# Optimization experiments

Hardware: AMD Instinct MI355X
Metric: run time of the kernel (lower is better)

The kernel has to match this reference:

```python
import jax, jax.numpy as jnp
import numpy as np

B, N, C = 2, 2048, 768
H, HD = 12, 64
HID = 3072
LN_EPS = 1e-5
POL_EPS = 1e-6


def _layer_norm(x, g, b):
    m = jnp.mean(x, axis=-1, keepdims=True)
    v = jnp.mean(jnp.square(x - m), axis=-1, keepdims=True)
    return (x - m) * jax.lax.rsqrt(v + LN_EPS) * g + b


def _softmax_with_policy(attn, policy):
    # attn: [B,H,N,N], policy: [B,N,1]
    n = attn.shape[-1]
    ap = policy.reshape(policy.shape[0], 1, 1, n)  # [B,1,1,N]
    eye = jnp.eye(n, dtype=ap.dtype)[None, None]   # [1,1,N,N]
    ap = ap + (1.0 - ap) * eye                     # always attend to self
    attn = attn - jnp.max(attn, axis=-1, keepdims=True)
    attn = jnp.exp(attn.astype(jnp.float32)) * ap.astype(jnp.float32)
    attn = (attn + POL_EPS / n) / (jnp.sum(attn, axis=-1, keepdims=True) + POL_EPS)
    return attn


def setup_inputs() -> dict:
    key = jax.random.key(0)
    ks = jax.random.split(key, 12)
    s = lambda fan_in: 1.0 / np.sqrt(fan_in)
    x = jax.random.normal(ks[0], (B, N, C), dtype=jnp.float32)
    policy = (jax.random.uniform(ks[1], (B, N, 1)) > 0.5).astype(jnp.float32)
    return {
        "x": x,
        "policy": policy,
        "ln1_g": jnp.ones((C,), jnp.float32),
        "ln1_b": jnp.zeros((C,), jnp.float32),
        "qkv_w": jax.random.uniform(ks[2], (3 * H * HD, C), jnp.float32, -s(C), s(C)),
        "proj_w": jax.random.uniform(ks[3], (C, H * HD), jnp.float32, -s(H * HD), s(H * HD)),
        "proj_b": jnp.zeros((C,), jnp.float32),
        "ln2_g": jnp.ones((C,), jnp.float32),
        "ln2_b": jnp.zeros((C,), jnp.float32),
        "fc1_w": jax.random.uniform(ks[4], (HID, C), jnp.float32, -s(C), s(C)),
        "fc1_b": jnp.zeros((HID,), jnp.float32),
        "fc2_w": jax.random.uniform(ks[5], (C, HID), jnp.float32, -s(HID), s(HID)),
        "fc2_b": jnp.zeros((C,), jnp.float32),
    }


def reference(x, policy, ln1_g, ln1_b, qkv_w, proj_w, proj_b, ln2_g, ln2_b, fc1_w, fc1_b, fc2_w, fc2_b):
    b, n, c = x.shape
    scale = HD ** -0.5
    # --- attention branch (pre-LN) ---
    h = _layer_norm(x, ln1_g, ln1_b)
    qkv = (h @ qkv_w.T).reshape(b, n, 3, H, HD).transpose(2, 0, 3, 1, 4)  # [3,B,H,N,hd]
    q, k, v = qkv[0], qkv[1], qkv[2]
    attn = jnp.einsum("bhqd,bhkd->bhqk", q * scale, k)
    attn = _softmax_with_policy(attn, policy).astype(x.dtype)
    o = jnp.einsum("bhqk,bhkd->bhqd", attn, v).transpose(0, 2, 1, 3).reshape(b, n, H * HD)
    x = x + (o @ proj_w.T + proj_b)  # skip_lam = 1.0, dropout/drop_path = identity
    # --- MLP branch (pre-LN) ---
    h = _layer_norm(x, ln2_g, ln2_b)
    h = jax.nn.gelu(h @ fc1_w.T + fc1_b, approximate=False)  # torch nn.GELU = exact erf
    x = x + (h @ fc2_w.T + fc2_b)
    return x
```

## Files before the change

### kernel.cpp

```cpp
#include <hip/hip_runtime.h>

typedef unsigned short u16;
typedef unsigned int u32;
typedef float f32x4 __attribute__((ext_vector_type(4)));
typedef float f32x16 __attribute__((ext_vector_type(16)));
typedef __bf16 bf16x8 __attribute__((ext_vector_type(8)));
typedef u16 u16x4v __attribute__((ext_vector_type(4)));
typedef u32 u32x2 __attribute__((ext_vector_type(2)));
typedef u32 u32x4 __attribute__((ext_vector_type(4)));

#define NHEAD 12
#define NN 2048
#define CC 768

#define GLOBAL_AS __attribute__((address_space(1)))
#define LDS_AS __attribute__((address_space(3)))

__device__ __forceinline__ u16 tobf(float f) {
  __bf16 h = (__bf16)f;
  return __builtin_bit_cast(u16, h);
}
__device__ __forceinline__ float bf2f(u16 h) {
  u32 u = ((u32)h) << 16;
  return __builtin_bit_cast(float, u);
}
__device__ __forceinline__ void plswap(u32& a, u32& b) {
  asm volatile("v_permlane32_swap_b32 %0, %1" : "+v"(a), "+v"(b));
}
__device__ __forceinline__ void plswapf(float& a, float& b) {
  asm volatile("v_permlane32_swap_b32 %0, %1" : "+v"(a), "+v"(b));
}

#define N4_QKV 442368
#define N4_PROJ 147456
#define N4_FC 589824
__global__ __launch_bounds__(256) void cvt4_kernel(
    const float* __restrict__ a, const float* __restrict__ b,
    const float* __restrict__ c, const float* __restrict__ d,
    u16* __restrict__ oa, u16* __restrict__ ob, u16* __restrict__ oc,
    u16* __restrict__ od) {
  int i = blockIdx.x * 256 + threadIdx.x;
  const float* src;
  u16* dst;
  if (i < N4_QKV) {
    src = a; dst = oa;
  } else if (i < N4_QKV + N4_PROJ) {
    i -= N4_QKV; src = b; dst = ob;
  } else if (i < N4_QKV + N4_PROJ + N4_FC) {
    i -= N4_QKV + N4_PROJ; src = c; dst = oc;
  } else {
    i -= N4_QKV + N4_PROJ + N4_FC; src = d; dst = od;
    if (i >= N4_FC) return;
  }
  float4 v = ((const float4*)src)[i];
  u16x4v o = {tobf(v.x), tobf(v.y), tobf(v.z), tobf(v.w)};
  ((u16x4v*)dst)[i] = o;
}

__global__ __launch_bounds__(256) void ln_kernel(const float* __restrict__ x,
                                                 const float* __restrict__ gw,
                                                 const float* __restrict__ bw,
                                                 u16* __restrict__ out) {
  int row = blockIdx.x * 4 + (threadIdx.x >> 6);
  int lane = threadIdx.x & 63;
  const float* xr = x + (size_t)row * CC + lane * 12;
  float v[12];
  *(float4*)&v[0] = *(const float4*)(xr + 0);
  *(float4*)&v[4] = *(const float4*)(xr + 4);
  *(float4*)&v[8] = *(const float4*)(xr + 8);
  float s = 0.f, sq = 0.f;
#pragma unroll
  for (int j = 0; j < 12; ++j) { s += v[j]; sq += v[j] * v[j]; }
#pragma unroll
  for (int o = 1; o < 64; o <<= 1) { s += __shfl_xor(s, o); sq += __shfl_xor(sq, o); }
  float mean = s * (1.f / CC);
  float var = sq * (1.f / CC) - mean * mean;
  float rs = rsqrtf(var + 1e-5f);
  u16 ob[12];
#pragma unroll
  for (int j = 0; j < 12; ++j) {
    int c = lane * 12 + j;
    ob[j] = tobf((v[j] - mean) * rs * gw[c] + bw[c]);
  }
  u32* orow = (u32*)(out + (size_t)row * CC + lane * 12);
#pragma unroll
  for (int j = 0; j < 6; ++j) orow[j] = (u32)ob[2 * j] | ((u32)ob[2 * j + 1] << 16);
}

template <int BM, int OB, int HASB, int ACT, int RES>
__global__ __launch_bounds__(256) void gemm_kernel(
    const u16* __restrict__ A, const u16* __restrict__ Bw,
    const float* __restrict__ bias, const float* __restrict__ res,
    void* __restrict__ Cout, int M, int N, int K) {
  constexpr int MW = BM / 2;
  constexpr int MF = MW / 16;
  __shared__ __align__(16) u16 Alds[BM * 64];
  __shared__ __align__(16) u16 Blds[128 * 64];
  const int tid = threadIdx.x;
  const int lane = tid & 63, wave = tid >> 6;
  const int l15 = lane & 15, g = lane >> 4;
  const int bm = blockIdx.x * BM, bn = blockIdx.y * 128;
  const int wm = (wave >> 1) * MW, wn = (wave & 1) * 64;
  f32x4 acc[MF][4] = {};

  for (int kt = 0; kt < K; kt += 64) {
#pragma unroll
    for (int i = 0; i < BM / 32; ++i) {
      int ob_ = i * 4096 + wave * 1024;
      int lb = ob_ + lane * 16;
      int row = lb >> 7;
      int cb = (lb & 127) ^ ((row & 7) << 4);
      const u16* sa = A + (size_t)(bm + row) * K + kt + (cb >> 1);
      __builtin_amdgcn_global_load_lds((const GLOBAL_AS void*)sa,
                                       (LDS_AS void*)(Alds + (ob_ >> 1)), 16, 0, 0);
    }
#pragma unroll
    for (int i = 0; i < 4; ++i) {
      int ob_ = i * 4096 + wave * 1024;
      int lb = ob_ + lane * 16;
      int row = lb >> 7;
      int cb = (lb & 127) ^ ((row & 7) << 4);
      const u16* sb = Bw + (size_t)(bn + row) * K + kt + (cb >> 1);
      __builtin_amdgcn_global_load_lds((const GLOBAL_AS void*)sb,
                                       (LDS_AS void*)(Blds + (ob_ >> 1)), 16, 0, 0);
    }
    __syncthreads();
#pragma unroll
    for (int ks = 0; ks < 2; ++ks) {
      bf16x8 af[MF], bfr[4];
#pragma unroll
      for (int mi = 0; mi < MF; ++mi) {
        int row = wm + mi * 16 + l15;
        int cb = (ks * 64 + g * 16) ^ ((row & 7) << 4);
        af[mi] = *(const bf16x8*)&Alds[row * 64 + (cb >> 1)];
      }
#pragma unroll
      for (int ni = 0; ni < 4; ++ni) {
        int row = wn + ni * 16 + l15;
        int cb = (ks * 64 + g * 16) ^ ((row & 7) << 4);
        bfr[ni] = *(const bf16x8*)&Blds[row * 64 + (cb >> 1)];
      }
#pragma unroll
      for (int mi = 0; mi < MF; ++mi)
#pragma unroll
        for (int ni = 0; ni < 4; ++ni)
          acc[mi][ni] = __builtin_amdgcn_mfma_f32_16x16x32_bf16(af[mi], bfr[ni],
                                                                acc[mi][ni], 0, 0, 0);
    }
    __syncthreads();
  }
#pragma unroll
  for (int mi = 0; mi < MF; ++mi) {
#pragma unroll
    for (int ni = 0; ni < 4; ++ni) {
      int col = bn + wn + ni * 16 + l15;
      float bs = HASB ? bias[col] : 0.f;
#pragma unroll
      for (int r = 0; r < 4; ++r) {
        int rowm = bm + wm + mi * 16 + g * 4 + r;
        float v = acc[mi][ni][r] + bs;
        if (ACT) v = 0.5f * v * (1.f + erff(v * 0.70710678118654752f));
        if (RES) v += res[(size_t)rowm * N + col];
        if (OB)
          ((u16*)Cout)[(size_t)rowm * N + col] = tobf(v);
        else
          ((float*)Cout)[(size_t)rowm * N + col] = v;
      }
    }
  }
}

__global__ __launch_bounds__(256) void vsum_kernel(const u16* __restrict__ qkv,
                                                   float* __restrict__ vs) {
  int bh = blockIdx.x, q4 = blockIdx.y;
  int b = bh / NHEAD, h = bh % NHEAD;
  int d = threadIdx.x & 63, part = threadIdx.x >> 6;
  float s = 0.f;
  for (int n = q4 * 512 + part; n < q4 * 512 + 512; n += 4)
    s += bf2f(qkv[(size_t)(b * NN + n) * 2304 + 2 * CC + h * 64 + d]);
  __shared__ float red[256];
  red[threadIdx.x] = s;
  __syncthreads();
  if (threadIdx.x < 64) {
    float t = red[threadIdx.x] + red[threadIdx.x + 64] + red[threadIdx.x + 128] +
              red[threadIdx.x + 192];
    vs[q4 * (24 * 64) + bh * 64 + threadIdx.x] = t;
  }
}

#define SCL2E 0.18033688f
#define TRRD(dst, addr, OFF) \
  asm volatile("ds_read_b64_tr_b16 %0, %1 offset:" OFF : "=v"(dst) : "v"(addr))
#define VMW(N)                                          \
  asm volatile("s_waitcnt vmcnt(" #N ")" ::: "memory"); \
  __builtin_amdgcn_sched_barrier(0);

__global__ __launch_bounds__(256) void attn32_kernel(const u16* __restrict__ qkv,
                                                     const float* __restrict__ policy,
                                                     float* __restrict__ partO,
                                                     float* __restrict__ partlm) {
  __shared__ __align__(16) u16 Vlds[4][2][2048];
  __shared__ u16 PolB[NN];
  __shared__ float alf[4][32];
  const int bh = blockIdx.y, b = bh / NHEAD, h = bh % NHEAD;
  const int qt = blockIdx.x >> 1, half = blockIdx.x & 1;
  const int tid = threadIdx.x, lane = tid & 63, w = tid >> 6;
  const int l31 = lane & 31, hp = lane >> 5, b4 = (lane >> 4) & 1, l15 = lane & 15;
  const int q0 = qt * 128 + w * 32;
  const int kv0 = half * 1024;

  bf16x8 qf0, qf1, qf2, qf3;
  {
    const u16* qp = qkv + (size_t)(b * NN + q0 + l31) * 2304 + h * 64 + 8 * hp;
#pragma unroll
    for (int ds = 0; ds < 4; ++ds) {
      bf16x8 r = *(const bf16x8*)(qp + ds * 16);
      bf16x8 o;
#pragma unroll
      for (int j = 0; j < 8; ++j) o[j] = (__bf16)((float)r[j] * SCL2E);
      if (ds == 0) qf0 = o; else if (ds == 1) qf1 = o; else if (ds == 2) qf2 = o; else qf3 = o;
    }
  }

  const u16* kptr = qkv + (size_t)(b * NN + kv0 + l31) * 2304 + CC + h * 64 + 8 * hp;
  const u16* vsrc[4];
#pragma unroll
  for (int c = 0; c < 4; ++c) {
    int L = c * 64 + lane;
    int idx0 = L * 8;
    int s0 = idx0 & 15, jj = (idx0 >> 4) & 3, b4v = (idx0 >> 6) & 1,
        pv = (idx0 >> 7) & 1, hv = (idx0 >> 8) & 1, dtv = (idx0 >> 9) & 1,
        mkv = (idx0 >> 10) & 1;
    int key = mkv * 16 + 8 * hv + 4 * pv + jj;
    int d0 = dtv * 32 + 16 * b4v + s0;
    vsrc[c] = qkv + (size_t)(b * NN + kv0 + key) * 2304 + 2 * CC + h * 64 + d0;
  }

#define LOADK(R0, R1, R2, R3)              \
  {                                        \
    R0 = *(const bf16x8*)(kptr);           \
    R1 = *(const bf16x8*)(kptr + 16);      \
    R2 = *(const bf16x8*)(kptr + 32);      \
    R3 = *(const bf16x8*)(kptr + 48);      \
    kptr += 73728;                         \
  }
#define STAGEV(BUF)                                                              \
  {                                                                              \
    _Pragma("unroll") for (int c = 0; c < 4; ++c) {                              \
      __builtin_amdgcn_global_load_lds((const GLOBAL_AS void*)vsrc[c],           \
                                       (LDS_AS void*)&Vlds[w][BUF][c * 512], 16, \
                                       0, 0);                                    \
      vsrc[c] += 73728;                                                          \
    }                                                                            \
  }

  bf16x8 kA0, kA1, kA2, kA3, kB0, kB1, kB2, kB3;
  STAGEV(0);
  LOADK(kA0, kA1, kA2, kA3);
  {
    float4 p0 = *(const float4*)&policy[b * NN + tid * 8];
    float4 p1 = *(const float4*)&policy[b * NN + tid * 8 + 4];
    u16x4v a = {tobf(p0.x), tobf(p0.y), tobf(p0.z), tobf(p0.w)};
    u16x4v c2 = {tobf(p1.x), tobf(p1.y), tobf(p1.z), tobf(p1.w)};
    *(u16x4v*)&PolB[tid * 8] = a;
    *(u16x4v*)&PolB[tid * 8 + 4] = c2;
  }
  __syncthreads();

  float m_cur = -3.0e38f, m_true = -3.0e38f, l_run = 0.f;
  f32x16 accd[2] = {};
  const u32 vwb = (u32)(uintptr_t)(LDS_AS u16*)&Vlds[w][0][0] +
                  (u32)(2 * l15 + 128 * b4 + 512 * hp);

  auto tile_body = [&](int T, bf16x8 k0, bf16x8 k1, bf16x8 k2, bf16x8 k3,
                       int bufb) {
    f32x16 sv = {};
    sv = __builtin_amdgcn_mfma_f32_32x32x16_bf16(k0, qf0, sv, 0, 0, 0);
    sv = __builtin_amdgcn_mfma_f32_32x32x16_bf16(k1, qf1, sv, 0, 0, 0);
    sv = __builtin_amdgcn_mfma_f32_32x32x16_bf16(k2, qf2, sv, 0, 0, 0);
    sv = __builtin_amdgcn_mfma_f32_32x32x16_bf16(k3, qf3, sv, 0, 0, 0);

    u32x2 t00a, t00b, t01a, t01b, t10a, t10b, t11a, t11b;
    {
      u32 vab = vwb + (u32)(bufb * 4096);
      TRRD(t00a, vab, "0");    TRRD(t00b, vab, "256");
      TRRD(t01a, vab, "1024"); TRRD(t01b, vab, "1280");
      TRRD(t10a, vab, "2048"); TRRD(t10b, vab, "2304");
      TRRD(t11a, vab, "3072"); TRRD(t11b, vab, "3328");
    }

    float m01 = fmaxf(sv[0], sv[1]), m23 = fmaxf(sv[2], sv[3]);
    float m45 = fmaxf(sv[4], sv[5]), m67 = fmaxf(sv[6], sv[7]);
    float m89 = fmaxf(sv[8], sv[9]), mab = fmaxf(sv[10], sv[11]);
    float mcd = fmaxf(sv[12], sv[13]), mef = fmaxf(sv[14], sv[15]);
    float tmax = fmaxf(fmaxf(fmaxf(m01, m23), fmaxf(m45, m67)),
                       fmaxf(fmaxf(m89, mab), fmaxf(mcd, mef)));
    {
      float t1 = tmax, t2 = tmax;
      plswapf(t1, t2);
      tmax = fmaxf(t1, t2);
    }
    m_true = fmaxf(m_true, tmax);
    const bool defer = __all(tmax <= m_cur + 8.f);
    const float m_new = defer ? m_cur : fmaxf(m_cur, tmax);

    const int kvg = kv0 + T * 32;
    const bool isdiag = (kvg == q0);
    u16 pb[16];
    float psum = 0.f;
#pragma unroll
    for (int i = 0; i < 4; ++i) {
      u16x4v pq = *(const u16x4v*)&PolB[kvg + 8 * i + 4 * hp];
#pragma unroll
      for (int rq = 0; rq < 4; ++rq) {
        int r = 4 * i + rq;
        float ap = bf2f(pq[rq]);
        if (isdiag) ap = ((8 * i + 4 * hp + rq) == l31) ? 1.f : ap;
        float e = exp2f(sv[r] - m_new) * ap;
        u16 eb = tobf(e);
        psum += bf2f(eb);
        pb[r] = eb;
      }
    }
    {
      float s1 = psum, s2 = psum;
      plswapf(s1, s2);
      psum = s1 + s2;
    }
    if (!defer) {
      float alpha = exp2f(m_cur - m_new);
      l_run = l_run * alpha + psum;
      m_cur = m_new;
      if (lane < 32) alf[w][lane] = alpha;
      float4 aq0 = *(const float4*)&alf[w][4 * hp];
      float4 aq1 = *(const float4*)&alf[w][8 + 4 * hp];
      float4 aq2 = *(const float4*)&alf[w][16 + 4 * hp];
      float4 aq3 = *(const float4*)&alf[w][24 + 4 * hp];
#pragma unroll
      for (int dt = 0; dt < 2; ++dt) {
#pragma unroll
        for (int rq = 0; rq < 4; ++rq) {
          accd[dt][0 + rq] *= ((const float*)&aq0)[rq];
          accd[dt][4 + rq] *= ((const float*)&aq1)[rq];
          accd[dt][8 + rq] *= ((const float*)&aq2)[rq];
          accd[dt][12 + rq] *= ((const float*)&aq3)[rq];
        }
      }
    } else {
      l_run += psum;
    }

    u32 PK0[4], PK1[4];
    PK0[0] = (u32)pb[0] | ((u32)pb[1] << 16);
    PK0[1] = (u32)pb[2] | ((u32)pb[3] << 16);
    PK0[2] = (u32)pb[4] | ((u32)pb[5] << 16);
    PK0[3] = (u32)pb[6] | ((u32)pb[7] << 16);
    PK1[0] = (u32)pb[8] | ((u32)pb[9] << 16);
    PK1[1] = (u32)pb[10] | ((u32)pb[11] << 16);
    PK1[2] = (u32)pb[12] | ((u32)pb[13] << 16);
    PK1[3] = (u32)pb[14] | ((u32)pb[15] << 16);
    plswap(PK0[2], PK0[0]);
    plswap(PK0[3], PK0[1]);
    plswap(PK1[2], PK1[0]);
    plswap(PK1[3], PK1[1]);

    asm volatile("s_waitcnt lgkmcnt(0)" ::: "memory");
    __builtin_amdgcn_sched_barrier(0);

    {
      u32x4 p4 = {PK0[0], PK0[1], PK0[2], PK0[3]};
      bf16x8 pf = __builtin_bit_cast(bf16x8, p4);
      u32x4 v0 = {t00a.x, t00a.y, t00b.x, t00b.y};
      u32x4 v1 = {t01a.x, t01a.y, t01b.x, t01b.y};
      accd[0] = __builtin_amdgcn_mfma_f32_32x32x16_bf16(
          pf, __builtin_bit_cast(bf16x8, v0), accd[0], 0, 0, 0);
      accd[1] = __builtin_amdgcn_mfma_f32_32x32x16_bf16(
          pf, __builtin_bit_cast(bf16x8, v1), accd[1], 0, 0, 0);
    }
    {
      u32x4 p4 = {PK1[0], PK1[1], PK1[2], PK1[3]};
      bf16x8 pf = __builtin_bit_cast(bf16x8, p4);
      u32x4 v0 = {t10a.x, t10a.y, t10b.x, t10b.y};
      u32x4 v1 = {t11a.x, t11a.y, t11b.x, t11b.y};
      accd[0] = __builtin_amdgcn_mfma_f32_32x32x16_bf16(
          pf, __builtin_bit_cast(bf16x8, v0), accd[0], 0, 0, 0);
      accd[1] = __builtin_amdgcn_mfma_f32_32x32x16_bf16(
          pf, __builtin_bit_cast(bf16x8, v1), accd[1], 0, 0, 0);
    }
  };

  for (int tt = 0; tt < 16; ++tt) {
    LOADK(kB0, kB1, kB2, kB3);
    STAGEV(1);
    VMW(8);
    tile_body(2 * tt, kA0, kA1, kA2, kA3, 0);
    if (tt < 15) {
      LOADK(kA0, kA1, kA2, kA3);
      STAGEV(0);
      VMW(8);
    } else {
      VMW(0);
    }
    tile_body(2 * tt + 1, kB0, kB1, kB2, kB3, 1);
  }

  float sr = exp2f(m_cur - m_true);
  if (lane < 32) {
    alf[w][lane] = sr;
    float2 lm = {l_run * sr, m_true};
    *(float2*)&partlm[2 * ((size_t)(half * 24 + bh) * 2048 + q0 + lane)] = lm;
  }
  float4 sq0 = *(const float4*)&alf[w][4 * hp];
  float4 sq1 = *(const float4*)&alf[w][8 + 4 * hp];
  float4 sq2 = *(const float4*)&alf[w][16 + 4 * hp];
  float4 sq3 = *(const float4*)&alf[w][24 + 4 * hp];
  float* pb2 = partO + ((size_t)(half * 24 + bh) * 2048) * 64;
#pragma unroll
  for (int dt = 0; dt < 2; ++dt) {
#pragma unroll
    for (int i = 0; i < 4; ++i) {
      float4 sqv = (i == 0) ? sq0 : (i == 1) ? sq1 : (i == 2) ? sq2 : sq3;
#pragma unroll
      for (int rq = 0; rq < 4; ++rq) {
        int row = q0 + 8 * i + 4 * hp + rq;
        pb2[(size_t)row * 64 + dt * 32 + l31] = accd[dt][4 * i + rq] * ((const float*)&sqv)[rq];
      }
    }
  }
#undef LOADK
#undef STAGEV
}

__global__ __launch_bounds__(256) void merge_kernel(const float* __restrict__ partO,
                                                    const float* __restrict__ partlm,
                                                    const float* __restrict__ vs,
                                                    u16* __restrict__ o) {
  int rr = blockIdx.x * 4 + (threadIdx.x >> 6);
  int lane = threadIdx.x & 63;
  int bh = rr >> 11, q = rr & 2047;
  int b = bh / NHEAD, h = bh % NHEAD;
  const float* O1 = partO + ((size_t)bh * 2048 + q) * 64;
  const float* O2 = partO + ((size_t)(24 + bh) * 2048 + q) * 64;
  float2 lm1 = ((const float2*)partlm)[(size_t)bh * 2048 + q];
  float2 lm2 = ((const float2*)partlm)[(size_t)(24 + bh) * 2048 + q];
  float ms = fmaxf(lm1.y, lm2.y);
  float w1 = exp2f(lm1.y - ms), w2 = exp2f(lm2.y - ms);
  float den = lm1.x * w1 + lm2.x * w2 + 1e-6f;
  float vsv = vs[bh * 64 + lane] + vs[1536 + bh * 64 + lane] +
              vs[3072 + bh * 64 + lane] + vs[4608 + bh * 64 + lane];
  float num = O1[lane] * w1 + O2[lane] * w2 + (1e-6f / 2048.f) * vsv;
  o[((size_t)(b * NN + q)) * CC + h * 64 + lane] = tobf(num / den);
}

extern "C" void kernel_launch(void* const* d_in, const int* in_sizes, int n_in,
                              void* d_out, int out_size, void* d_ws, size_t ws_size,
                              hipStream_t stream) {
  const float* x = (const float*)d_in[0];
  const float* policy = (const float*)d_in[1];
  const float* ln1g = (const float*)d_in[2];
  const float* ln1b = (const float*)d_in[3];
  const float* qkvw = (const float*)d_in[4];
  const float* projw = (const float*)d_in[5];
  const float* projb = (const float*)d_in[6];
  const float* ln2g = (const float*)d_in[7];
  const float* ln2b = (const float*)d_in[8];
  const float* fc1w = (const float*)d_in[9];
  const float* fc1b = (const float*)d_in[10];
  const float* fc2w = (const float*)d_in[11];
  const float* fc2b = (const float*)d_in[12];
  float* out = (float*)d_out;

  char* ws = (char*)d_ws;
  size_t off = 0;
  auto alloc = [&](size_t bytes) {
    void* p = ws + off;
    off = (off + bytes + 255) & ~(size_t)255;
    return p;
  };
  u16* wq = (u16*)alloc((size_t)2304 * 768 * 2);
  u16* wp = (u16*)alloc((size_t)768 * 768 * 2);
  u16* w1 = (u16*)alloc((size_t)3072 * 768 * 2);
  u16* w2 = (u16*)alloc((size_t)768 * 3072 * 2);
  u16* hbuf = (u16*)alloc((size_t)4096 * 768 * 2);
  u16* qkv = (u16*)alloc((size_t)4096 * 2304 * 2);
  u16* obuf = (u16*)alloc((size_t)4096 * 768 * 2);
  float* vs = (float*)alloc((size_t)4 * 24 * 64 * 4);
  size_t unionOff = off;
  float* partO = (float*)alloc((size_t)2 * 24 * 2048 * 64 * 4);
  float* partlm = (float*)alloc((size_t)2 * 24 * 2048 * 2 * 4);
  float* x1 = (float*)(ws + unionOff);
  u16* f1 = qkv;

  cvt4_kernel<<<6912, 256, 0, stream>>>(qkvw, projw, fc1w, fc2w, wq, wp, w1, w2);

  ln_kernel<<<1024, 256, 0, stream>>>(x, ln1g, ln1b, hbuf);
  gemm_kernel<128, 1, 0, 0, 0><<<dim3(32, 18), 256, 0, stream>>>(
      hbuf, wq, nullptr, nullptr, qkv, 4096, 2304, 768);
  vsum_kernel<<<dim3(24, 4), 256, 0, stream>>>(qkv, vs);
  attn32_kernel<<<dim3(32, 24), 256, 0, stream>>>(qkv, policy, partO, partlm);
  merge_kernel<<<12288, 256, 0, stream>>>(partO, partlm, vs, obuf);
  gemm_kernel<64, 0, 1, 0, 1><<<dim3(64, 6), 256, 0, stream>>>(
      obuf, wp, projb, x, x1, 4096, 768, 768);
  ln_kernel<<<1024, 256, 0, stream>>>(x1, ln2g, ln2b, hbuf);
  gemm_kernel<128, 1, 1, 1, 0><<<dim3(32, 24), 256, 0, stream>>>(
      hbuf, w1, fc1b, nullptr, f1, 4096, 3072, 768);
  gemm_kernel<64, 0, 1, 0, 1><<<dim3(64, 6), 256, 0, stream>>>(
      f1, w2, fc2b, x1, out, 4096, 768, 3072);
}
```

Measured before the change: 263.8 us.

## Swizzle GEMM tile order and streamline attention softmax conversions

The GEMM kernel remaps block indices through a modulo-8 swizzle, probably to spread neighbouring tiles across XCDs or improve L2 reuse. In the attention kernel, policy values are kept as fp32 in LDS. The kernel now uses the raw hardware exp2 instruction and packs bf16 pairs with v_cvt_pk_bf16_f32 instead of per-element conversion and shifting. It also reshapes the max reduction tree and forces the main KV loop not to unroll, which lowers code size and register pressure but may cost some scheduling freedom.

```diff
diff --git a/kernel.cpp b/kernel.cpp
--- a/kernel.cpp
+++ b/kernel.cpp
@@ -23,6 +23,11 @@
 __device__ __forceinline__ float bf2f(u16 h) {
   u32 u = ((u32)h) << 16;
   return __builtin_bit_cast(float, u);
+}
+__device__ __forceinline__ u32 cvtpk(float lo, float hi) {
+  u32 r;
+  asm("v_cvt_pk_bf16_f32 %0, %1, %2" : "=v"(r) : "v"(lo), "v"(hi));
+  return r;
 }
 __device__ __forceinline__ void plswap(u32& a, u32& b) {
   asm volatile("v_permlane32_swap_b32 %0, %1" : "+v"(a), "+v"(b));
@@ -99,7 +104,11 @@
   const int tid = threadIdx.x;
   const int lane = tid & 63, wave = tid >> 6;
   const int l15 = lane & 15, g = lane >> 4;
-  const int bm = blockIdx.x * BM, bn = blockIdx.y * 128;
+  const int nx = gridDim.x;
+  const int flat = blockIdx.y * nx + blockIdx.x;
+  const int cpx = (nx * gridDim.y) >> 3;
+  const int swz = (flat & 7) * cpx + (flat >> 3);
+  const int bm = (swz % nx) * BM, bn = (swz / nx) * 128;
   const int wm = (wave >> 1) * MW, wn = (wave & 1) * 64;
   f32x4 acc[MF][4] = {};
 
@@ -200,7 +209,7 @@
                                                      float* __restrict__ partO,
                                                      float* __restrict__ partlm) {
   __shared__ __align__(16) u16 Vlds[4][2][2048];
-  __shared__ u16 PolB[NN];
+  __shared__ float PolF[NN];
   __shared__ float alf[4][32];
   const int bh = blockIdx.y, b = bh / NHEAD, h = bh % NHEAD;
   const int qt = blockIdx.x >> 1, half = blockIdx.x & 1;
@@ -260,10 +269,8 @@
   {
     float4 p0 = *(const float4*)&policy[b * NN + tid * 8];
     float4 p1 = *(const float4*)&policy[b * NN + tid * 8 + 4];
-    u16x4v a = {tobf(p0.x), tobf(p0.y), tobf(p0.z), tobf(p0.w)};
-    u16x4v c2 = {tobf(p1.x), tobf(p1.y), tobf(p1.z), tobf(p1.w)};
-    *(u16x4v*)&PolB[tid * 8] = a;
-    *(u16x4v*)&PolB[tid * 8 + 4] = c2;
+    *(float4*)&PolF[tid * 8] = p0;
+    *(float4*)&PolF[tid * 8 + 4] = p1;
   }
   __syncthreads();
 
@@ -272,8 +279,8 @@
   const u32 vwb = (u32)(uintptr_t)(LDS_AS u16*)&Vlds[w][0][0] +
                   (u32)(2 * l15 + 128 * b4 + 512 * hp);
 
-  auto tile_body = [&](int T, bf16x8 k0, bf16x8 k1, bf16x8 k2, bf16x8 k3,
-                       int bufb) {
+  auto tile_body = [&](int T, const bf16x8& k0, const bf16x8& k1,
+                       const bf16x8& k2, const bf16x8& k3, int bufb) {
     f32x16 sv = {};
     sv = __builtin_amdgcn_mfma_f32_32x32x16_bf16(k0, qf0, sv, 0, 0, 0);
     sv = __builtin_amdgcn_mfma_f32_32x32x16_bf16(k1, qf1, sv, 0, 0, 0);
@@ -289,12 +296,12 @@
       TRRD(t11a, vab, "3072"); TRRD(t11b, vab, "3328");
     }
 
-    float m01 = fmaxf(sv[0], sv[1]), m23 = fmaxf(sv[2], sv[3]);
-    float m45 = fmaxf(sv[4], sv[5]), m67 = fmaxf(sv[6], sv[7]);
-    float m89 = fmaxf(sv[8], sv[9]), mab = fmaxf(sv[10], sv[11]);
-    float mcd = fmaxf(sv[12], sv[13]), mef = fmaxf(sv[14], sv[15]);
-    float tmax = fmaxf(fmaxf(fmaxf(m01, m23), fmaxf(m45, m67)),
-                       fmaxf(fmaxf(m89, mab), fmaxf(mcd, mef)));
+    float ta = fmaxf(fmaxf(sv[0], sv[1]), sv[2]);
+    float tb = fmaxf(fmaxf(sv[3], sv[4]), sv[5]);
+    float tc = fmaxf(fmaxf(sv[6], sv[7]), sv[8]);
+    float td = fmaxf(fmaxf(sv[9], sv[10]), sv[11]);
+    float te = fmaxf(fmaxf(sv[12], sv[13]), sv[14]);
+    float tmax = fmaxf(fmaxf(fmaxf(ta, tb), tc), fmaxf(fmaxf(td, te), sv[15]));
     {
       float t1 = tmax, t2 = tmax;
       plswapf(t1, t2);
@@ -306,21 +313,26 @@
 
     const int kvg = kv0 + T * 32;
     const bool isdiag = (kvg == q0);
-    u16 pb[16];
-    float psum = 0.f;
+    float ev[16];
 #pragma unroll
     for (int i = 0; i < 4; ++i) {
-      u16x4v pq = *(const u16x4v*)&PolB[kvg + 8 * i + 4 * hp];
+      float4 pq = *(const float4*)&PolF[kvg + 8 * i + 4 * hp];
 #pragma unroll
       for (int rq = 0; rq < 4; ++rq) {
         int r = 4 * i + rq;
-        float ap = bf2f(pq[rq]);
+        float ap = ((const float*)&pq)[rq];
         if (isdiag) ap = ((8 * i + 4 * hp + rq) == l31) ? 1.f : ap;
-        float e = exp2f(sv[r] - m_new) * ap;
-        u16 eb = tobf(e);
-        psum += bf2f(eb);
-        pb[r] = eb;
+        ev[r] = __builtin_amdgcn_exp2f(sv[r] - m_new) * ap;
       }
+    }
+    u32 wv[8];
+#pragma unroll
+    for (int j = 0; j < 8; ++j) wv[j] = cvtpk(ev[2 * j], ev[2 * j + 1]);
+    float psum = 0.f;
+#pragma unroll
+    for (int j = 0; j < 8; ++j) {
+      psum += __builtin_bit_cast(float, wv[j] << 16);
+      psum += __builtin_bit_cast(float, wv[j] & 0xffff0000u);
     }
     {
       float s1 = psum, s2 = psum;
@@ -328,7 +340,7 @@
       psum = s1 + s2;
     }
     if (!defer) {
-      float alpha = exp2f(m_cur - m_new);
+      float alpha = __builtin_amdgcn_exp2f(m_cur - m_new);
       l_run = l_run * alpha + psum;
       m_cur = m_new;
       if (lane < 32) alf[w][lane] = alpha;
@@ -350,15 +362,8 @@
       l_run += psum;
     }
 
-    u32 PK0[4], PK1[4];
-    PK0[0] = (u32)pb[0] | ((u32)pb[1] << 16);
-    PK0[1] = (u32)pb[2] | ((u32)pb[3] << 16);
-    PK0[2] = (u32)pb[4] | ((u32)pb[5] << 16);
-    PK0[3] = (u32)pb[6] | ((u32)pb[7] << 16);
-    PK1[0] = (u32)pb[8] | ((u32)pb[9] << 16);
-    PK1[1] = (u32)pb[10] | ((u32)pb[11] << 16);
-    PK1[2] = (u32)pb[12] | ((u32)pb[13] << 16);
-    PK1[3] = (u32)pb[14] | ((u32)pb[15] << 16);
+    u32 PK0[4] = {wv[0], wv[1], wv[2], wv[3]};
+    u32 PK1[4] = {wv[4], wv[5], wv[6], wv[7]};
     plswap(PK0[2], PK0[0]);
     plswap(PK0[3], PK0[1]);
     plswap(PK1[2], PK1[0]);
@@ -389,6 +394,7 @@
     }
   };
 
+#pragma unroll 1
   for (int tt = 0; tt < 16; ++tt) {
     LOADK(kB0, kB1, kB2, kB3);
     STAGEV(1);
@@ -404,7 +410,7 @@
     tile_body(2 * tt + 1, kB0, kB1, kB2, kB3, 1);
   }
 
-  float sr = exp2f(m_cur - m_true);
+  float sr = __builtin_amdgcn_exp2f(m_cur - m_true);
   if (lane < 32) {
     alf[w][lane] = sr;
     float2 lm = {l_run * sr, m_true};
```

Measured after the change: 260.3 us. No clear change (-1.3%).
